# Kernel optimization log

Measured on AMD Instinct MI355X. Metric: run time of the kernel, lower is better.

The kernel has to match this reference:

```python
import jax, jax.numpy as jnp
import numpy as np

K = 4
G = 64
IN_DIM = 256
OUT_DIM = 256
BATCH = 512
T0, T1 = -1.0, 1.0


def setup_inputs() -> dict:
    key = jax.random.key(0)
    kx, kw = jax.random.split(key)
    x = jax.random.uniform(kx, (BATCH, IN_DIM), jnp.float32, T0, T1)
    # xavier_normal_ on [G+K, in, out]: std = sqrt(2 / (fan_in + fan_out)) with fan over last two dims
    std = (2.0 / (IN_DIM + OUT_DIM)) ** 0.5
    w = jax.random.normal(kw, (G + K, IN_DIM, OUT_DIM), jnp.float32) * std
    # knot vector: k-1 repeats of t0, linspace(t0,t1,G+1), k-1 repeats of t1
    t = jnp.concatenate([
        jnp.full((K - 1,), T0, jnp.float32),
        jnp.linspace(T0, T1, G + 1, dtype=jnp.float32),
        jnp.full((K - 1,), T1, jnp.float32),
    ])
    return {"x": x, "w": w, "t": t, "k": K}


def _basis(x, t, k):
    """Cox-de Boor: the k nonzero order-k B-spline basis values at each x.
    Returns (idx, N): idx [..., k] basis indices i-k+1..i, N [..., k] values."""
    n_t = t.shape[0]
    # interval i with t[i] <= x < t[i+1], clipped to the valid span
    i = jnp.clip(jnp.searchsorted(t, x, side='right') - 1, k - 1, n_t - k - 1)
    N = jnp.ones(x.shape + (1,), x.dtype)
    for p in range(1, k):  # static small loop (k=4)
        jj = jnp.arange(1, p + 1)
        left = x[..., None] - t[i[..., None] + 1 - jj]   # [..., p]
        right = t[i[..., None] + jj] - x[..., None]      # [..., p]
        saved = jnp.zeros_like(x)
        vals = []
        for r in range(p):
            d = right[..., r] + left[..., p - 1 - r]      # t[i+r+1] - t[i+r+1-p]
            temp = N[..., r] / d
            vals.append(saved + right[..., r] * temp)
            saved = left[..., p - 1 - r] * temp
        vals.append(saved)
        N = jnp.stack(vals, -1)
    idx = i[..., None] - (k - 1) + jnp.arange(k)
    return idx, N


def reference(x, w, t, k):
    in_dim = x.shape[1]
    n_rows = w.shape[0]
    idx, y1 = _basis(x, t, k)                             # [B,in,k], [B,in,k]
    # last row of w (index -1 == n_rows-1) weights the SiLU residual term
    idx_full = jnp.concatenate(
        [idx, jnp.full(idx.shape[:-1] + (1,), n_rows - 1, idx.dtype)], -1)  # [B,in,k+1]
    silu = x * jax.nn.sigmoid(x)
    y2 = jnp.concatenate([y1, silu[..., None]], -1)       # [B,in,k+1]
    # gather local spline coefficients: w2[b,c,j,o] = w[idx_full[b,c,j], c, o]
    w2 = w[idx_full, jnp.arange(in_dim)[None, :, None], :]  # [B,in,k+1,out]
    return jnp.einsum('bcjo,bcj->bo', w2, y2)             # [B,out]
```

## Files before the change

### kernel.cpp

```cpp
#include <hip/hip_runtime.h>
#include <hip/hip_fp16.h>
#include <math.h>
#include <stdint.h>

#define IN_DIM  256
#define OUT_DIM 256
#define NROWS   68
#define NT      71
#define BATCH   512
#define KPAD    96
#define NCG     32
#define PART_FLOATS (NCG * BATCH * OUT_DIM)
#define WB_SHORTS   (IN_DIM * OUT_DIM * KPAD)

typedef _Float16 f16x8 __attribute__((ext_vector_type(8)));
typedef float    f32x4 __attribute__((ext_vector_type(4)));

__global__ __launch_bounds__(256) void cvt_kernel(const float* __restrict__ w,
                                                  unsigned short* __restrict__ wb) {
  __shared__ unsigned short l16[NROWS][64];
  const int c  = blockIdx.x >> 2;
  const int ot = (blockIdx.x & 3) << 6;
  const int t  = threadIdx.x;
  const int o1 = t & 63, k0 = t >> 6;
  for (int k = k0; k < NROWS; k += 4) {
    const float v = w[((size_t)k * IN_DIM + c) * OUT_DIM + ot + o1];
    l16[k][o1] = __half_as_ushort(__float2half_rn(v));
  }
  __syncthreads();
  #pragma unroll
  for (int i = 0; i < 3; ++i) {
    const int u = t + 256 * i;
    const int o2 = u / 12, seg = u % 12, k8 = seg * 8;
    uint32_t hl[4];
    #pragma unroll
    for (int j = 0; j < 4; ++j) {
      const int ka = k8 + 2 * j, kb = ka + 1;
      const uint32_t lo = (ka < NROWS) ? l16[ka][o2] : 0u;
      const uint32_t hi = (kb < NROWS) ? l16[kb][o2] : 0u;
      hl[j] = lo | (hi << 16);
    }
    *(uint4*)(wb + ((size_t)(c * 256 + ot + o2) * KPAD + k8)) =
        make_uint4(hl[0], hl[1], hl[2], hl[3]);
  }
}

__global__ __launch_bounds__(256) void kan_gather_kernel(
    const float* __restrict__ x, const unsigned short* __restrict__ wbu,
    const float* __restrict__ t, float* __restrict__ part) {
  __shared__ uint4 Wb[2][3072];
  __shared__ unsigned short Ylds[64 * 104];
  __shared__ float4 nA[8][64];
  __shared__ float  sA[8][64];
  __shared__ int    bA[8][64];
  __shared__ float  lt[NT];

  const int tid   = threadIdx.x;
  const int cg    = blockIdx.x & 31;
  const int btile = blockIdx.x >> 5;
  const int wv    = tid >> 6;
  const int lane  = tid & 63;
  const int m16   = lane & 15;
  const int g16b  = (lane >> 4) * 16;

  if (tid < NT) lt[tid] = t[tid];
  __syncthreads();

  {
    const char* src0 = (const char*)wbu + (size_t)(cg * 8 + 0) * 49152;
    #pragma unroll
    for (int j = 0; j < 12; ++j) {
      const int s = wv * 12 + j;
      __builtin_amdgcn_global_load_lds((const uint32_t*)(src0 + s * 1024 + lane * 16),
                                       (uint32_t*)(&Wb[0][s * 64]), 16, 0, 0);
    }
  }

  for (int p = tid; p < 512; p += 256) {
    const int c = p >> 6, bb = p & 63;
    const float xv = x[(size_t)(btile * 64 + bb) * IN_DIM + cg * 8 + c];
    int i = 3 + (int)floorf((xv + 1.0f) * 32.0f);
    i = i < 3 ? 3 : (i > 66 ? 66 : i);
    while (i > 3 && xv < lt[i]) --i;
    while (i < 66 && xv >= lt[i + 1]) ++i;
    float N0 = 1.f, N1 = 0.f, N2 = 0.f, N3 = 0.f;
    { const float l1 = xv - lt[i], r1 = lt[i + 1] - xv;
      const float tp = N0 / (r1 + l1); N1 = l1 * tp; N0 = r1 * tp; }
    { const float l1 = xv - lt[i], l2 = xv - lt[i - 1];
      const float r1 = lt[i + 1] - xv, r2 = lt[i + 2] - xv;
      float saved = 0.f;
      const float tp0 = N0 / (r1 + l2); const float n0 = saved + r1 * tp0; saved = l2 * tp0;
      const float tp1 = N1 / (r2 + l1); const float n1 = saved + r2 * tp1; saved = l1 * tp1;
      N0 = n0; N1 = n1; N2 = saved; }
    { const float l1 = xv - lt[i], l2 = xv - lt[i - 1], l3 = xv - lt[i - 2];
      const float r1 = lt[i + 1] - xv, r2 = lt[i + 2] - xv, r3 = lt[i + 3] - xv;
      float saved = 0.f;
      const float tp0 = N0 / (r1 + l3); const float n0 = saved + r1 * tp0; saved = l3 * tp0;
      const float tp1 = N1 / (r2 + l2); const float n1 = saved + r2 * tp1; saved = l2 * tp1;
      const float tp2 = N2 / (r3 + l1); const float n2 = saved + r3 * tp2; saved = l1 * tp2;
      N0 = n0; N1 = n1; N2 = n2; N3 = saved; }
    nA[c][bb] = make_float4(N0, N1, N2, N3);
    sA[c][bb] = xv / (1.0f + expf(-xv));
    bA[c][bb] = i - 3;
  }
  __syncthreads();

  f32x4 acc[4][4];
  #pragma unroll
  for (int a = 0; a < 4; ++a)
    #pragma unroll
    for (int b = 0; b < 4; ++b) acc[a][b] = f32x4{0.f, 0.f, 0.f, 0.f};

  for (int ch = 0; ch < 8; ++ch) {
    for (int i = tid; i < 1664; i += 256)
      *(uint2*)((char*)Ylds + (size_t)i * 8) = make_uint2(0u, 0u);
    __syncthreads();
    if (tid < 64) {
      const int bb = tid;
      unsigned short* yr = &Ylds[bb * 104];
      const float4 yv = nA[ch][bb];
      const int base = bA[ch][bb];
      yr[base + 0] = __half_as_ushort(__float2half_rn(yv.x));
      yr[base + 1] = __half_as_ushort(__float2half_rn(yv.y));
      yr[base + 2] = __half_as_ushort(__float2half_rn(yv.z));
      yr[base + 3] = __half_as_ushort(__float2half_rn(yv.w));
      yr[67]       = __half_as_ushort(__float2half_rn(sA[ch][bb]));
    }
    __syncthreads();

    if (ch < 7) {
      const char* srcN = (const char*)wbu + (size_t)(cg * 8 + ch + 1) * 49152;
      uint4* dstN = &Wb[(ch + 1) & 1][0];
      #pragma unroll
      for (int j = 0; j < 12; ++j) {
        const int s = wv * 12 + j;
        __builtin_amdgcn_global_load_lds((const uint32_t*)(srcN + s * 1024 + lane * 16),
                                         (uint32_t*)(dstN + s * 64), 16, 0, 0);
      }
    }

    const char* Wc = (const char*)&Wb[ch & 1][0];
    #pragma unroll
    for (int kb = 0; kb < 3; ++kb) {
      f16x8 af[4];
      #pragma unroll
      for (int ot = 0; ot < 4; ++ot) {
        const int o = wv * 64 + ot * 16 + m16;
        af[ot] = *(const f16x8*)(Wc + o * 192 + kb * 64 + g16b);
      }
      #pragma unroll
      for (int bt = 0; bt < 4; ++bt) {
        const f16x8 bf = *(const f16x8*)((const char*)Ylds + (bt * 16 + m16) * 208 + kb * 64 + g16b);
        #pragma unroll
        for (int ot = 0; ot < 4; ++ot)
          acc[ot][bt] = __builtin_amdgcn_mfma_f32_16x16x32_f16(af[ot], bf, acc[ot][bt], 0, 0, 0);
      }
    }
    __syncthreads();
  }

  float* bounce = (float*)&Wb[0][0];
  #pragma unroll
  for (int ot = 0; ot < 4; ++ot)
    #pragma unroll
    for (int bt = 0; bt < 4; ++bt)
      #pragma unroll
      for (int r = 0; r < 4; ++r) {
        const int o = wv * 64 + ot * 16 + (lane >> 4) * 4 + r;
        const int b = bt * 16 + m16;
        bounce[b * 260 + o] = acc[ot][bt][r];
      }
  __syncthreads();
  #pragma unroll
  for (int i = 0; i < 16; ++i) {
    const int idx = tid + 256 * i;
    const int b = idx >> 6, o4 = (idx & 63) * 4;
    const float4 v = *(const float4*)&bounce[b * 260 + o4];
    *(float4*)(part + ((size_t)cg * BATCH + btile * 64 + b) * OUT_DIM + o4) = v;
  }
}

__global__ __launch_bounds__(256) void reduce_kernel(const float* __restrict__ part,
                                                     float* __restrict__ out) {
  const int q = blockIdx.x * 256 + threadIdx.x;
  const int S = BATCH * OUT_DIM / 4;
  const float4* p = (const float4*)part;
  float4 s = p[q];
  #pragma unroll
  for (int k = 1; k < NCG; ++k) {
    const float4 a = p[q + k * S];
    s.x += a.x; s.y += a.y; s.z += a.z; s.w += a.w;
  }
  ((float4*)out)[q] = s;
}

extern "C" void kernel_launch(void* const* d_in, const int* in_sizes, int n_in,
                              void* d_out, int out_size, void* d_ws, size_t ws_size,
                              hipStream_t stream) {
  const float* x = (const float*)d_in[0];
  const float* w = (const float*)d_in[1];
  const float* t = (const float*)d_in[2];
  float* out  = (float*)d_out;
  float* part = (float*)d_ws;
  unsigned short* wb = (unsigned short*)((float*)d_ws + PART_FLOATS);
  cvt_kernel<<<1024, 256, 0, stream>>>(w, wb);
  kan_gather_kernel<<<256, 256, 0, stream>>>(x, wb, t, part);
  reduce_kernel<<<BATCH * OUT_DIM / 4 / 256, 256, 0, stream>>>(part, out);
}
```

Measured before the change: 100.1 us.

## Load weight fragments directly to registers and double wave count per block

The fp16 weight layout becomes MFMA-fragment-major, so each wave loads its A fragments straight from global memory into registers, replacing the double-buffered LDS staging. The gather kernel now runs 512 threads with 8 waves, each covering 32 outputs. The Y tile is zeroed once, and each channel step clears only the four previously written entries instead of re-zeroing the whole tile, which removes one barrier per channel. The conversion kernel now uses one block per input channel with float4 loads. The cost is that global load latency is no longer hidden by LDS prefetch across channels.

```diff
diff --git a/kernel.cpp b/kernel.cpp
--- a/kernel.cpp
+++ b/kernel.cpp
@@ -18,66 +18,65 @@
 
 __global__ __launch_bounds__(256) void cvt_kernel(const float* __restrict__ w,
                                                   unsigned short* __restrict__ wb) {
-  __shared__ unsigned short l16[NROWS][64];
-  const int c  = blockIdx.x >> 2;
-  const int ot = (blockIdx.x & 3) << 6;
-  const int t  = threadIdx.x;
-  const int o1 = t & 63, k0 = t >> 6;
-  for (int k = k0; k < NROWS; k += 4) {
-    const float v = w[((size_t)k * IN_DIM + c) * OUT_DIM + ot + o1];
-    l16[k][o1] = __half_as_ushort(__float2half_rn(v));
+  __shared__ unsigned short l16[NROWS][264];
+  const int c = blockIdx.x;
+  const int t = threadIdx.x;
+  const int o4 = (t & 63) * 4;
+  for (int k = (t >> 6); k < NROWS; k += 4) {
+    const float4 v = *(const float4*)(w + ((size_t)k * IN_DIM + c) * OUT_DIM + o4);
+    l16[k][o4 + 0] = __half_as_ushort(__float2half_rn(v.x));
+    l16[k][o4 + 1] = __half_as_ushort(__float2half_rn(v.y));
+    l16[k][o4 + 2] = __half_as_ushort(__float2half_rn(v.z));
+    l16[k][o4 + 3] = __half_as_ushort(__float2half_rn(v.w));
   }
   __syncthreads();
   #pragma unroll
-  for (int i = 0; i < 3; ++i) {
-    const int u = t + 256 * i;
-    const int o2 = u / 12, seg = u % 12, k8 = seg * 8;
+  for (int i = 0; i < 12; ++i) {
+    const int idx = t + 256 * i;
+    const int kb  = idx >> 10;
+    const int o   = (idx >> 2) & 255;
+    const int g   = idx & 3;
+    const int k8  = kb * 32 + g * 8;
     uint32_t hl[4];
     #pragma unroll
     for (int j = 0; j < 4; ++j) {
-      const int ka = k8 + 2 * j, kb = ka + 1;
-      const uint32_t lo = (ka < NROWS) ? l16[ka][o2] : 0u;
-      const uint32_t hi = (kb < NROWS) ? l16[kb][o2] : 0u;
+      const int ka = k8 + 2 * j, k2 = ka + 1;
+      const uint32_t lo = (ka < NROWS) ? (uint32_t)l16[ka][o] : 0u;
+      const uint32_t hi = (k2 < NROWS) ? (uint32_t)l16[k2][o] : 0u;
       hl[j] = lo | (hi << 16);
     }
-    *(uint4*)(wb + ((size_t)(c * 256 + ot + o2) * KPAD + k8)) =
+    *(uint4*)(wb + (((size_t)(c * 3 + kb) * 256 + o) * 32 + g * 8)) =
         make_uint4(hl[0], hl[1], hl[2], hl[3]);
   }
 }
 
-__global__ __launch_bounds__(256) void kan_gather_kernel(
+__global__ __launch_bounds__(512) void kan_gather_kernel(
     const float* __restrict__ x, const unsigned short* __restrict__ wbu,
     const float* __restrict__ t, float* __restrict__ part) {
-  __shared__ uint4 Wb[2][3072];
-  __shared__ unsigned short Ylds[64 * 104];
+  __shared__ float  lt[NT];
+  __shared__ uint4  YldsRaw[832];
   __shared__ float4 nA[8][64];
   __shared__ float  sA[8][64];
   __shared__ int    bA[8][64];
-  __shared__ float  lt[NT];
+  __shared__ float  bounce[64 * 260];
 
+  unsigned short* Ylds = (unsigned short*)YldsRaw;
   const int tid   = threadIdx.x;
   const int cg    = blockIdx.x & 31;
   const int btile = blockIdx.x >> 5;
   const int wv    = tid >> 6;
   const int lane  = tid & 63;
   const int m16   = lane & 15;
-  const int g16b  = (lane >> 4) * 16;
+  const int g     = lane >> 4;
+  const int ob    = wv * 32;
 
   if (tid < NT) lt[tid] = t[tid];
+  for (int i = tid; i < 832; i += 512)
+    YldsRaw[i] = make_uint4(0u, 0u, 0u, 0u);
   __syncthreads();
 
   {
-    const char* src0 = (const char*)wbu + (size_t)(cg * 8 + 0) * 49152;
-    #pragma unroll
-    for (int j = 0; j < 12; ++j) {
-      const int s = wv * 12 + j;
-      __builtin_amdgcn_global_load_lds((const uint32_t*)(src0 + s * 1024 + lane * 16),
-                                       (uint32_t*)(&Wb[0][s * 64]), 16, 0, 0);
-    }
-  }
-
-  for (int p = tid; p < 512; p += 256) {
-    const int c = p >> 6, bb = p & 63;
+    const int c = tid >> 6, bb = tid & 63;
     const float xv = x[(size_t)(btile * 64 + bb) * IN_DIM + cg * 8 + c];
     int i = 3 + (int)floorf((xv + 1.0f) * 32.0f);
     i = i < 3 ? 3 : (i > 66 ? 66 : i);
@@ -105,78 +104,69 @@
   }
   __syncthreads();
 
-  f32x4 acc[4][4];
+  const uint4* wbu4 = (const uint4*)wbu;
+  f32x4 acc[2][4];
   #pragma unroll
-  for (int a = 0; a < 4; ++a)
+  for (int ot = 0; ot < 2; ++ot)
     #pragma unroll
-    for (int b = 0; b < 4; ++b) acc[a][b] = f32x4{0.f, 0.f, 0.f, 0.f};
+    for (int bt = 0; bt < 4; ++bt) acc[ot][bt] = f32x4{0.f, 0.f, 0.f, 0.f};
 
+  int prevb = -1;
   for (int ch = 0; ch < 8; ++ch) {
-    for (int i = tid; i < 1664; i += 256)
-      *(uint2*)((char*)Ylds + (size_t)i * 8) = make_uint2(0u, 0u);
-    __syncthreads();
     if (tid < 64) {
-      const int bb = tid;
-      unsigned short* yr = &Ylds[bb * 104];
-      const float4 yv = nA[ch][bb];
-      const int base = bA[ch][bb];
+      unsigned short* yr = Ylds + tid * 104;
+      if (prevb >= 0) {
+        yr[prevb + 0] = 0; yr[prevb + 1] = 0; yr[prevb + 2] = 0; yr[prevb + 3] = 0;
+      }
+      const float4 yv = nA[ch][tid];
+      const int base = bA[ch][tid];
       yr[base + 0] = __half_as_ushort(__float2half_rn(yv.x));
       yr[base + 1] = __half_as_ushort(__float2half_rn(yv.y));
       yr[base + 2] = __half_as_ushort(__float2half_rn(yv.z));
       yr[base + 3] = __half_as_ushort(__float2half_rn(yv.w));
-      yr[67]       = __half_as_ushort(__float2half_rn(sA[ch][bb]));
+      yr[67]       = __half_as_ushort(__float2half_rn(sA[ch][tid]));
+      prevb = base;
+    }
+    uint4 af[6];
+    {
+      const int c3 = (cg * 8 + ch) * 3;
+      #pragma unroll
+      for (int ot = 0; ot < 2; ++ot)
+        #pragma unroll
+        for (int kb = 0; kb < 3; ++kb)
+          af[ot * 3 + kb] =
+              wbu4[((size_t)(c3 + kb) * 256 + ob + ot * 16 + m16) * 4 + g];
     }
     __syncthreads();
 
-    if (ch < 7) {
-      const char* srcN = (const char*)wbu + (size_t)(cg * 8 + ch + 1) * 49152;
-      uint4* dstN = &Wb[(ch + 1) & 1][0];
-      #pragma unroll
-      for (int j = 0; j < 12; ++j) {
-        const int s = wv * 12 + j;
-        __builtin_amdgcn_global_load_lds((const uint32_t*)(srcN + s * 1024 + lane * 16),
-                                         (uint32_t*)(dstN + s * 64), 16, 0, 0);
-      }
-    }
-
-    const char* Wc = (const char*)&Wb[ch & 1][0];
     #pragma unroll
     for (int kb = 0; kb < 3; ++kb) {
-      f16x8 af[4];
-      #pragma unroll
-      for (int ot = 0; ot < 4; ++ot) {
-        const int o = wv * 64 + ot * 16 + m16;
-        af[ot] = *(const f16x8*)(Wc + o * 192 + kb * 64 + g16b);
-      }
       #pragma unroll
       for (int bt = 0; bt < 4; ++bt) {
-        const f16x8 bf = *(const f16x8*)((const char*)Ylds + (bt * 16 + m16) * 208 + kb * 64 + g16b);
-        #pragma unroll
-        for (int ot = 0; ot < 4; ++ot)
-          acc[ot][bt] = __builtin_amdgcn_mfma_f32_16x16x32_f16(af[ot], bf, acc[ot][bt], 0, 0, 0);
+        const f16x8 bf = *(const f16x8*)(Ylds + (bt * 16 + m16) * 104 + kb * 32 + g * 8);
+        acc[0][bt] = __builtin_amdgcn_mfma_f32_16x16x32_f16(
+            __builtin_bit_cast(f16x8, af[0 * 3 + kb]), bf, acc[0][bt], 0, 0, 0);
+        acc[1][bt] = __builtin_amdgcn_mfma_f32_16x16x32_f16(
+            __builtin_bit_cast(f16x8, af[1 * 3 + kb]), bf, acc[1][bt], 0, 0, 0);
       }
     }
     __syncthreads();
   }
 
-  float* bounce = (float*)&Wb[0][0];
   #pragma unroll
-  for (int ot = 0; ot < 4; ++ot)
+  for (int ot = 0; ot < 2; ++ot)
     #pragma unroll
     for (int bt = 0; bt < 4; ++bt)
       #pragma unroll
-      for (int r = 0; r < 4; ++r) {
-        const int o = wv * 64 + ot * 16 + (lane >> 4) * 4 + r;
-        const int b = bt * 16 + m16;
-        bounce[b * 260 + o] = acc[ot][bt][r];
-      }
+      for (int r = 0; r < 4; ++r)
+        bounce[(bt * 16 + m16) * 260 + ob + ot * 16 + g * 4 + r] = acc[ot][bt][r];
   __syncthreads();
   #pragma unroll
-  for (int i = 0; i < 16; ++i) {
-    const int idx = tid + 256 * i;
+  for (int i = 0; i < 8; ++i) {
+    const int idx = tid + 512 * i;
     const int b = idx >> 6, o4 = (idx & 63) * 4;
-    const float4 v = *(const float4*)&bounce[b * 260 + o4];
-    *(float4*)(part + ((size_t)cg * BATCH + btile * 64 + b) * OUT_DIM + o4) = v;
+    *(float4*)(part + ((size_t)cg * BATCH + btile * 64 + b) * OUT_DIM + o4) =
+        *(const float4*)(bounce + b * 260 + o4);
   }
 }
 
@@ -203,7 +193,7 @@
   float* out  = (float*)d_out;
   float* part = (float*)d_ws;
   unsigned short* wb = (unsigned short*)((float*)d_ws + PART_FLOATS);
-  cvt_kernel<<<1024, 256, 0, stream>>>(w, wb);
-  kan_gather_kernel<<<256, 256, 0, stream>>>(x, wb, t, part);
+  cvt_kernel<<<IN_DIM, 256, 0, stream>>>(w, wb);
+  kan_gather_kernel<<<256, 512, 0, stream>>>(x, wb, t, part);
   reduce_kernel<<<BATCH * OUT_DIM / 4 / 256, 256, 0, stream>>>(part, out);
 }
```

Measured after the change: 96.99 us. 1.03x faster.
